# Optimization experiments

Hardware: AMD Instinct MI355X
Metric: run time of the kernel (lower is better)

The kernel has to match this reference:

```python
import jax, jax.numpy as jnp
import numpy as np

S, B, I, H, NQ = 256, 64, 512, 1024, 4


def setup_inputs() -> dict:
    key = jax.random.key(0)
    ks = jax.random.split(key, 12)
    w = lambda k, sh: jax.random.normal(k, sh, jnp.float32) * 0.05
    return {
        "inputs": jax.random.normal(ks[0], (S, B, I), jnp.float32),
        "Wf": w(ks[1], (I + H, H)), "bf": jnp.zeros((H,), jnp.float32),
        "Wi": w(ks[2], (I + H, H)), "bi": jnp.zeros((H,), jnp.float32),
        "Wu": w(ks[3], (I + H, H)), "bu": jnp.zeros((H,), jnp.float32),
        "Wo": w(ks[4], (I + H, H)), "bo": jnp.zeros((H,), jnp.float32),
        "pf": jax.random.normal(ks[5], (NQ,), jnp.float32),
        "pi_q": jax.random.normal(ks[6], (NQ,), jnp.float32),
        "pu": jax.random.normal(ks[7], (NQ,), jnp.float32),
        "po": jax.random.normal(ks[8], (NQ,), jnp.float32),
        "Wc": w(ks[9], (H + 1, H)), "bc": jnp.zeros((H,), jnp.float32),
    }


def reference(inputs, Wf, bf, Wi, bi, Wu, bu, Wo, bo, pf, pi_q, pu, po, Wc, bc):
    # inputs: (S, B, I); states initialized to zeros
    def qgate(pre, p):
        # pre: (B, H); use first NQ features -> simulated <Z> = cos(2*theta)
        theta = pre[:, :NQ] @ p  # (B,)
        return jnp.cos(2.0 * theta)[:, None]  # (B, 1)

    def comb(v):
        return v @ Wc + bc

    def step(carry, x):
        hx, cx = carry
        c = jnp.concatenate([x, hx], axis=1)  # (B, I+H)
        pre_f = c @ Wf + bf
        pre_i = c @ Wi + bi
        pre_u = c @ Wu + bu
        pre_o = c @ Wo + bo
        f = jax.nn.sigmoid(comb(jnp.concatenate(
            [jax.nn.sigmoid(pre_f), jax.nn.sigmoid(qgate(pre_f, pf))], axis=1)))
        i = jax.nn.sigmoid(comb(jnp.concatenate(
            [jax.nn.sigmoid(pre_i), jax.nn.sigmoid(qgate(pre_i, pi_q))], axis=1)))
        g = jnp.tanh(comb(jnp.concatenate(
            [jnp.tanh(pre_u), qgate(pre_u, pu)], axis=1)))  # update gate: no sigmoid on quantum part
        o = jax.nn.sigmoid(comb(jnp.concatenate(
            [jax.nn.sigmoid(pre_o), jax.nn.sigmoid(qgate(pre_o, po))], axis=1)))
        cx_new = f * cx + i * g
        hx_new = o * jnp.tanh(cx_new)
        return (hx_new, cx_new), hx_new

    init = (jnp.zeros((B, H), inputs.dtype), jnp.zeros((B, H), inputs.dtype))
    (hx, cx), outputs = jax.lax.scan(step, init, inputs)
    return outputs, (hx, cx)
```

## Files before the change

kernel.cpp:

```cpp
#include <hip/hip_runtime.h>

#define S_LEN 256
#define B_SZ 64
#define I_SZ 512
#define H_SZ 1024
#define NBLK 256

typedef __bf16 bf16x8 __attribute__((ext_vector_type(8)));
typedef float f32x4 __attribute__((ext_vector_type(4)));
typedef unsigned long long u64;

__device__ __forceinline__ float sigmoidf_(float x){ return 1.f/(1.f + expf(-x)); }

__device__ __forceinline__ u64 ld_cc64(const u64* p){
  return __hip_atomic_load(p, __ATOMIC_RELAXED, __HIP_MEMORY_SCOPE_AGENT);
}
__device__ __forceinline__ void st_cc16(__bf16* p, __bf16 v){
  unsigned short b = __builtin_bit_cast(unsigned short, v);
  __hip_atomic_store((unsigned short*)p, b, __ATOMIC_RELAXED, __HIP_MEMORY_SCOPE_AGENT);
}
__device__ __forceinline__ void st_cc32(float* p, float v){
  __hip_atomic_store(p, v, __ATOMIC_RELAXED, __HIP_MEMORY_SCOPE_AGENT);
}
__device__ __forceinline__ float ld_cc32f(const float* p){
  return __hip_atomic_load(p, __ATOMIC_RELAXED, __HIP_MEMORY_SCOPE_AGENT);
}


__global__ __launch_bounds__(64) void pack_w4_k(const float* __restrict__ Wf, const float* __restrict__ Wi,
                                                const float* __restrict__ Wu, const float* __restrict__ Wo,
                                                __bf16* __restrict__ W4p){
  int blk = blockIdx.x;
  int nt = blk / 48, kb = blk % 48;
  int l = threadIdx.x;
  int n = nt*16 + (l & 15);
  int g = n >> 10, h = n & 1023;
  const float* W = (g==0)?Wf:((g==1)?Wi:((g==2)?Wu:Wo));
  int k0 = kb*32 + ((l>>4)<<3);
  __bf16 tmp[8];
#pragma unroll
  for (int j=0;j<8;j++) tmp[j] = (__bf16)W[(size_t)(k0+j)*H_SZ + h];
  *reinterpret_cast<bf16x8*>(W4p + ((size_t)blk*64 + l)*8) = *reinterpret_cast<bf16x8*>(tmp);
}

__global__ __launch_bounds__(64) void pack_wc_k(const float* __restrict__ Wc, __bf16* __restrict__ Wcp){
  int blk = blockIdx.x;
  int nt = blk / 32, kb = blk % 32;
  int l = threadIdx.x;
  int n = nt*16 + (l & 15);
  int k0 = kb*32 + ((l>>4)<<3);
  __bf16 tmp[8];
#pragma unroll
  for (int j=0;j<8;j++) tmp[j] = (__bf16)Wc[(size_t)(k0+j)*H_SZ + n];
  *reinterpret_cast<bf16x8*>(Wcp + ((size_t)blk*64 + l)*8) = *reinterpret_cast<bf16x8*>(tmp);
}

__global__ __launch_bounds__(256) void pack_x_k(const float* __restrict__ x, __bf16* __restrict__ xF){
  int bid = blockIdx.x;
  int s = bid >> 2, mt = bid & 3;
#pragma unroll
  for (int j=0;j<4;j++){
    int G = j*256 + threadIdx.x;
    int kb = G >> 6, lane = G & 63;
    int b = mt*16 + (lane & 15);
    int k0 = kb*32 + ((lane>>4)<<3);
    const float* src = x + ((size_t)s*B_SZ + b)*I_SZ + k0;
    float4 v0 = *reinterpret_cast<const float4*>(src);
    float4 v1 = *reinterpret_cast<const float4*>(src+4);
    __bf16 t[8] = {(__bf16)v0.x,(__bf16)v0.y,(__bf16)v0.z,(__bf16)v0.w,
                   (__bf16)v1.x,(__bf16)v1.y,(__bf16)v1.z,(__bf16)v1.w};
    *reinterpret_cast<bf16x8*>(xF + ((size_t)bid*1024 + G)*8) = *reinterpret_cast<bf16x8*>(t);
  }
}

__global__ void init_h_k(__bf16* __restrict__ hxF){
  int i = blockIdx.x*blockDim.x + threadIdx.x;
  hxF[i] = (__bf16)0.f;
}

__device__ __forceinline__ void bar_arrive(unsigned* flags, unsigned target){
  asm volatile("" ::: "memory");
  __syncthreads();
  if (threadIdx.x == 0)
    __hip_atomic_store(&flags[blockIdx.x], target, __ATOMIC_RELAXED, __HIP_MEMORY_SCOPE_AGENT);
}
__device__ __forceinline__ void bar_wait(const unsigned* flags, unsigned target){
  if (threadIdx.x < 64){
    const u64* f = (const u64*)flags;
    int i0 = (int)threadIdx.x * 2;
    for(;;){
      u64 a = __hip_atomic_load(f+i0,   __ATOMIC_RELAXED, __HIP_MEMORY_SCOPE_AGENT);
      u64 b = __hip_atomic_load(f+i0+1, __ATOMIC_RELAXED, __HIP_MEMORY_SCOPE_AGENT);
      bool ok = ((unsigned)a >= target) && ((unsigned)(a>>32) >= target)
             && ((unsigned)b >= target) && ((unsigned)(b>>32) >= target);
      if (__all(ok)) break;
      __builtin_amdgcn_s_sleep(1);
    }
  }
  __syncthreads();
}


__global__ __launch_bounds__(256, 1) void qlstm_persist_k(
    const __bf16* __restrict__ xF,
    __bf16* hxF,
    const __bf16* __restrict__ W4p, const __bf16* __restrict__ Wcp,
    const float* __restrict__ bfv, const float* __restrict__ biv,
    const float* __restrict__ buv, const float* __restrict__ bov,
    const float* __restrict__ pf, const float* __restrict__ piq,
    const float* __restrict__ pu, const float* __restrict__ po,
    const float* __restrict__ WcLast, const float* __restrict__ bc,
    __bf16* actF, float* zact,
    float* __restrict__ out,
    unsigned* flags)
{
  __shared__ __align__(16) __bf16 ldsWc[2*32*64*8];
  __shared__ __align__(16) char ldsA[32768];
  __shared__ float gx[4][8][32];
  __shared__ float pre4[16][4];

  const int tid = threadIdx.x;
  const int bid = blockIdx.x;
  const int wave = tid >> 6;
  const int l = tid & 63;
  const int col = l & 15;
  const int kq = l >> 4;

  const int mt1 = bid >> 6;
  const int nt64 = bid & 63;
  const int nt16 = nt64*4 + wave;
  const int g1 = nt16 >> 6;
  const int h1 = (nt16*16 + col) & 1023;

  const int mt2 = bid >> 5;
  const int ht  = bid & 31;
  const int r2 = tid >> 5;
  const int c2 = tid & 31;
  const int b2 = mt2*8 + r2;
  const int h2 = ht*32 + c2;
  const int slot2 = kq*8 + (l & 7);

  bf16x8 wfrag[48];
  {
    const bf16x8* src = (const bf16x8*)(W4p + ((size_t)nt16*48*64 + (size_t)l)*8);
#pragma unroll
    for (int kb=0;kb<48;kb++) wfrag[kb] = src[(size_t)kb*64];
  }
  {
    const u64* src = (const u64*)(Wcp + (size_t)(ht*2)*32*64*8);
    u64* dst = (u64*)ldsWc;
    for (int i = tid; i < 8192; i += 256) dst[i] = src[i];
  }

  const float* bptr = (g1==0)?bfv:((g1==1)?biv:((g1==2)?buv:bov));
  const float bias1 = bptr[h1];
  const bool isU1 = (g1==2);
  const bool isQb = ((nt64 & 15) == 0);
  const int gq = nt64 >> 4;
  float pq0=0.f,pq1=0.f,pq2=0.f,pq3=0.f;
  if (isQb && wave==0){
    const float* pq = (gq==0)?pf:((gq==1)?piq:((gq==2)?pu:po));
    pq0=pq[0]; pq1=pq[1]; pq2=pq[2]; pq3=pq[3];
  }

  const float wl2 = WcLast[h2];
  const float bc2 = bc[h2];
  float creg = 0.f;

  const int laneh = (b2 & 15) + (((c2 >> 3) & 3) << 4);
  const size_t hei = ((size_t)((b2>>4)*32 + ht)*64 + laneh)*8 + (c2 & 7);

  __syncthreads();

  const size_t SBH = (size_t)S_LEN*B_SZ*H_SZ;

  for (int s = 0; s < S_LEN; ++s){
    {
      f32x4 acc[4] = {{0,0,0,0},{0,0,0,0},{0,0,0,0},{0,0,0,0}};
      const bf16x8* xp = (const bf16x8*)xF + (size_t)(s*4 + mt1)*1024 + l;
      {
        bf16x8 xf[8];
#pragma unroll
        for (int j=0;j<8;j++) xf[j] = xp[(size_t)j*64];
#pragma unroll
        for (int j=0;j<8;j++)
          acc[j&3] = __builtin_amdgcn_mfma_f32_16x16x32_bf16(xf[j], wfrag[j], acc[j&3], 0,0,0);
#pragma unroll
        for (int j=0;j<8;j++) xf[j] = xp[(size_t)(8+j)*64];
#pragma unroll
        for (int j=0;j<8;j++)
          acc[j&3] = __builtin_amdgcn_mfma_f32_16x16x32_bf16(xf[j], wfrag[8+j], acc[j&3], 0,0,0);
      }

      bar_wait(flags, (unsigned)(2*s));

      {
        const u64* hp = (const u64*)hxF + (size_t)mt1*4096;
        u64 slo[8], shi[8];
#pragma unroll
        for (int i=0;i<8;i++){
          int G = tid + 256*i;
          slo[i] = ld_cc64(hp + (size_t)G*2);
          shi[i] = ld_cc64(hp + (size_t)G*2 + 1);
        }
#pragma unroll
        for (int i=0;i<8;i++){
          int G = tid + 256*i;
          ulonglong2 v; v.x = slo[i]; v.y = shi[i];
          *reinterpret_cast<ulonglong2*>(ldsA + (size_t)G*16) = v;
        }
      }
      __syncthreads();

#pragma unroll
      for (int kb=0;kb<32;kb++){
        bf16x8 a = *reinterpret_cast<const bf16x8*>(ldsA + ((size_t)kb*64 + l)*16);
        acc[kb&3] = __builtin_amdgcn_mfma_f32_16x16x32_bf16(a, wfrag[16+kb], acc[kb&3], 0,0,0);
      }
      f32x4 r = (acc[0]+acc[1])+(acc[2]+acc[3]);
      float pr[4];
#pragma unroll
      for (int rr=0;rr<4;rr++){
        int brow = mt1*16 + (kq<<2) + rr;
        float p = r[rr] + bias1;
        pr[rr] = p;
        float a = isU1 ? tanhf(p) : sigmoidf_(p);
        size_t ei = (((size_t)(g1*8 + (brow>>3))*32 + (h1>>5))*32
                     + (size_t)((((h1>>3)&3)<<3) + (brow&7)))*8 + (h1&7);
        st_cc16(&actF[ei], (__bf16)a);
      }
      if (isQb && wave==0){
        if (col < 4){
#pragma unroll
          for (int rr=0;rr<4;rr++) pre4[(kq<<2)+rr][col] = pr[rr];
        }
        if (l < 16){
          float th = pre4[l][0]*pq0 + pre4[l][1]*pq1 + pre4[l][2]*pq2 + pre4[l][3]*pq3;
          float z = cosf(2.f*th);
          st_cc32(&zact[gq*B_SZ + mt1*16 + l], (gq==2) ? z : sigmoidf_(z));
        }
      }
    }

    bar_arrive(flags, (unsigned)(2*s+1));
    bar_wait(flags, (unsigned)(2*s+1));

    {
      float zf = ld_cc32f(&zact[      b2]);
      float zi = ld_cc32f(&zact[ 64 + b2]);
      float zu = ld_cc32f(&zact[128 + b2]);
      float zo = ld_cc32f(&zact[192 + b2]);

      const u64* ap = (const u64*)actF + (size_t)(wave*8 + mt2)*2048 + (size_t)slot2*2;
      const bf16x8* bf0 = (const bf16x8*)ldsWc + l;
      const bf16x8* bf1 = bf0 + 2048;
      f32x4 acc2[4] = {{0,0,0,0},{0,0,0,0},{0,0,0,0},{0,0,0,0}};
      u64 A0lo[8], A0hi[8], A1lo[8], A1hi[8];
#pragma unroll
      for (int i=0;i<8;i++){
        A0lo[i] = ld_cc64(ap + (size_t)i*64);
        A0hi[i] = ld_cc64(ap + (size_t)i*64 + 1);
      }
#pragma unroll
      for (int c=0;c<4;c++){
        u64* clo = (c&1) ? A1lo : A0lo;
        u64* chi = (c&1) ? A1hi : A0hi;
        u64* nlo = (c&1) ? A0lo : A1lo;
        u64* nhi = (c&1) ? A0hi : A1hi;
        if (c < 3){
#pragma unroll
          for (int i=0;i<8;i++){
            nlo[i] = ld_cc64(ap + (size_t)((c+1)*8 + i)*64);
            nhi[i] = ld_cc64(ap + (size_t)((c+1)*8 + i)*64 + 1);
          }
        }
#pragma unroll
        for (int i=0;i<8;i++){
          int kb = c*8 + i;
          union{u64 u[2]; bf16x8 v;} a; a.u[0]=clo[i]; a.u[1]=chi[i];
          acc2[kb&1]     = __builtin_amdgcn_mfma_f32_16x16x32_bf16(a.v, bf0[(size_t)kb*64], acc2[kb&1], 0,0,0);
          acc2[2+(kb&1)] = __builtin_amdgcn_mfma_f32_16x16x32_bf16(a.v, bf1[(size_t)kb*64], acc2[2+(kb&1)], 0,0,0);
        }
      }
      f32x4 rA = acc2[0]+acc2[1];
      f32x4 rB = acc2[2]+acc2[3];
#pragma unroll
      for (int rr=0;rr<4;rr++){
        int row = (kq<<2) + rr;
        if (row < 8){
          gx[wave][row][col]      = rA[rr];
          gx[wave][row][16 + col] = rB[rr];
        }
      }
      __syncthreads();

      float fg = sigmoidf_(gx[0][r2][c2] + bc2 + zf*wl2);
      float ig = sigmoidf_(gx[1][r2][c2] + bc2 + zi*wl2);
      float gg = tanhf(    gx[2][r2][c2] + bc2 + zu*wl2);
      float og = sigmoidf_(gx[3][r2][c2] + bc2 + zo*wl2);
      float cn = fg*creg + ig*gg;
      creg = cn;
      float hn = og*tanhf(cn);
      st_cc16(&hxF[hei], (__bf16)hn);
      size_t idx = (size_t)b2*H_SZ + h2;
      __builtin_nontemporal_store(hn, &out[(size_t)s*B_SZ*H_SZ + idx]);
      if (s == S_LEN-1){
        __builtin_nontemporal_store(hn, &out[SBH + idx]);
        __builtin_nontemporal_store(cn, &out[SBH + (size_t)B_SZ*H_SZ + idx]);
      }
    }

    bar_arrive(flags, (unsigned)(2*s+2));
  }
}


extern "C" void kernel_launch(void* const* d_in, const int* in_sizes, int n_in,
                              void* d_out, int out_size, void* d_ws, size_t ws_size,
                              hipStream_t stream){
  const float* inputs = (const float*)d_in[0];
  const float* Wf  = (const float*)d_in[1];
  const float* bf_ = (const float*)d_in[2];
  const float* Wi  = (const float*)d_in[3];
  const float* bi_ = (const float*)d_in[4];
  const float* Wu  = (const float*)d_in[5];
  const float* bu_ = (const float*)d_in[6];
  const float* Wo  = (const float*)d_in[7];
  const float* bo_ = (const float*)d_in[8];
  const float* pf  = (const float*)d_in[9];
  const float* piq = (const float*)d_in[10];
  const float* pu  = (const float*)d_in[11];
  const float* po  = (const float*)d_in[12];
  const float* Wc  = (const float*)d_in[13];
  const float* bc  = (const float*)d_in[14];
  float* out = (float*)d_out;

  __bf16* W4p = (__bf16*)d_ws;
  __bf16* Wcp = W4p + (size_t)256*48*64*8;
  __bf16* xF  = Wcp + (size_t)64*32*64*8;
  __bf16* actF = xF + (size_t)S_LEN*B_SZ*I_SZ;
  __bf16* hxF = actF + (size_t)4*B_SZ*H_SZ;
  float*  zact = (float*)(hxF + (size_t)B_SZ*H_SZ);
  unsigned* flags = (unsigned*)(zact + 256);

  pack_w4_k<<<256*48, 64, 0, stream>>>(Wf, Wi, Wu, Wo, W4p);
  pack_wc_k<<<64*32, 64, 0, stream>>>(Wc, Wcp);
  pack_x_k<<<S_LEN*4, 256, 0, stream>>>(inputs, xF);
  init_h_k<<<256, 256, 0, stream>>>(hxF);
  hipMemsetAsync(flags, 0, NBLK*sizeof(unsigned), stream);

  qlstm_persist_k<<<NBLK, 256, 0, stream>>>(
      xF, hxF, W4p, Wcp, bf_, bi_, bu_, bo_, pf, piq, pu, po,
      Wc + (size_t)H_SZ*H_SZ, bc, actF, zact, out, flags);
}
```

Baseline: 3.252 ms.

## Split grid barrier so phase-2 starts on first half of activations

Adds a three-phase per-step barrier. Blocks producing the second half of the gate activations signal early, once their hidden-state load is done. Phase-2 consumers begin the first half of their K-reduction after the intermediate barrier and wait for the full barrier only before reading the remaining activations. This is meant to overlap part of the combine GEMM with the tail of the gate GEMM and shorten the serial critical path per timestep. It also precomputes the activation store indices out of the loop. The change relies on an ordering assumption about which blocks write which activation halves, and it assumes that bar_wait/bar_arrive semantics (not shown) handle the new counter values correctly.

```diff
diff --git a/kernel.cpp b/kernel.cpp
--- a/kernel.cpp
+++ b/kernel.cpp
@@ -131,6 +131,7 @@
   const int nt16 = nt64*4 + wave;
   const int g1 = nt16 >> 6;
   const int h1 = (nt16*16 + col) & 1023;
+  const bool isHalfA = ((nt64 & 15) < 8);
 
   const int mt2 = bid >> 5;
   const int ht  = bid & 31;
@@ -167,6 +168,13 @@
   const float bc2 = bc[h2];
   float creg = 0.f;
 
+  size_t eis[4];
+#pragma unroll
+  for (int rr=0;rr<4;rr++){
+    int brow = mt1*16 + (kq<<2) + rr;
+    eis[rr] = (((size_t)(g1*8 + (brow>>3))*32 + (h1>>5))*32
+               + (size_t)((((h1>>3)&3)<<3) + (brow&7)))*8 + (h1&7);
+  }
   const int laneh = (b2 & 15) + (((c2 >> 3) & 3) << 4);
   const size_t hei = ((size_t)((b2>>4)*32 + ht)*64 + laneh)*8 + (c2 & 7);
 
@@ -175,6 +183,7 @@
   const size_t SBH = (size_t)S_LEN*B_SZ*H_SZ;
 
   for (int s = 0; s < S_LEN; ++s){
+    const unsigned T = 3u*(unsigned)s;
     {
       f32x4 acc[4] = {{0,0,0,0},{0,0,0,0},{0,0,0,0},{0,0,0,0}};
       const bf16x8* xp = (const bf16x8*)xF + (size_t)(s*4 + mt1)*1024 + l;
@@ -192,7 +201,7 @@
           acc[j&3] = __builtin_amdgcn_mfma_f32_16x16x32_bf16(xf[j], wfrag[8+j], acc[j&3], 0,0,0);
       }
 
-      bar_wait(flags, (unsigned)(2*s));
+      bar_wait(flags, T);
 
       {
         const u64* hp = (const u64*)hxF + (size_t)mt1*4096;
@@ -212,6 +221,9 @@
       }
       __syncthreads();
 
+      if (!isHalfA && tid == 0)
+        __hip_atomic_store(&flags[bid], T+1u, __ATOMIC_RELAXED, __HIP_MEMORY_SCOPE_AGENT);
+
 #pragma unroll
       for (int kb=0;kb<32;kb++){
         bf16x8 a = *reinterpret_cast<const bf16x8*>(ldsA + ((size_t)kb*64 + l)*16);
@@ -221,13 +233,10 @@
       float pr[4];
 #pragma unroll
       for (int rr=0;rr<4;rr++){
-        int brow = mt1*16 + (kq<<2) + rr;
         float p = r[rr] + bias1;
         pr[rr] = p;
         float a = isU1 ? tanhf(p) : sigmoidf_(p);
-        size_t ei = (((size_t)(g1*8 + (brow>>3))*32 + (h1>>5))*32
-                     + (size_t)((((h1>>3)&3)<<3) + (brow&7)))*8 + (h1&7);
-        st_cc16(&actF[ei], (__bf16)a);
+        st_cc16(&actF[eis[rr]], (__bf16)a);
       }
       if (isQb && wave==0){
         if (col < 4){
@@ -242,8 +251,8 @@
       }
     }
 
-    bar_arrive(flags, (unsigned)(2*s+1));
-    bar_wait(flags, (unsigned)(2*s+1));
+    bar_arrive(flags, T+2u);
+    bar_wait(flags, T+1u);
 
     {
       float zf = ld_cc32f(&zact[      b2]);
@@ -262,26 +271,51 @@
         A0hi[i] = ld_cc64(ap + (size_t)i*64 + 1);
       }
 #pragma unroll
-      for (int c=0;c<4;c++){
-        u64* clo = (c&1) ? A1lo : A0lo;
-        u64* chi = (c&1) ? A1hi : A0hi;
-        u64* nlo = (c&1) ? A0lo : A1lo;
-        u64* nhi = (c&1) ? A0hi : A1hi;
-        if (c < 3){
-#pragma unroll
-          for (int i=0;i<8;i++){
-            nlo[i] = ld_cc64(ap + (size_t)((c+1)*8 + i)*64);
-            nhi[i] = ld_cc64(ap + (size_t)((c+1)*8 + i)*64 + 1);
-          }
-        }
-#pragma unroll
-        for (int i=0;i<8;i++){
-          int kb = c*8 + i;
-          union{u64 u[2]; bf16x8 v;} a; a.u[0]=clo[i]; a.u[1]=chi[i];
-          acc2[kb&1]     = __builtin_amdgcn_mfma_f32_16x16x32_bf16(a.v, bf0[(size_t)kb*64], acc2[kb&1], 0,0,0);
-          acc2[2+(kb&1)] = __builtin_amdgcn_mfma_f32_16x16x32_bf16(a.v, bf1[(size_t)kb*64], acc2[2+(kb&1)], 0,0,0);
-        }
-      }
+      for (int i=0;i<8;i++){
+        A1lo[i] = ld_cc64(ap + (size_t)(8+i)*64);
+        A1hi[i] = ld_cc64(ap + (size_t)(8+i)*64 + 1);
+      }
+#pragma unroll
+      for (int i=0;i<8;i++){
+        union{u64 u[2]; bf16x8 v;} a; a.u[0]=A0lo[i]; a.u[1]=A0hi[i];
+        acc2[i&1]     = __builtin_amdgcn_mfma_f32_16x16x32_bf16(a.v, bf0[(size_t)i*64], acc2[i&1], 0,0,0);
+        acc2[2+(i&1)] = __builtin_amdgcn_mfma_f32_16x16x32_bf16(a.v, bf1[(size_t)i*64], acc2[2+(i&1)], 0,0,0);
+      }
+
+      bar_wait(flags, T+2u);
+
+#pragma unroll
+      for (int i=0;i<8;i++){
+        A0lo[i] = ld_cc64(ap + (size_t)(16+i)*64);
+        A0hi[i] = ld_cc64(ap + (size_t)(16+i)*64 + 1);
+      }
+#pragma unroll
+      for (int i=0;i<8;i++){
+        int kb = 8+i;
+        union{u64 u[2]; bf16x8 v;} a; a.u[0]=A1lo[i]; a.u[1]=A1hi[i];
+        acc2[kb&1]     = __builtin_amdgcn_mfma_f32_16x16x32_bf16(a.v, bf0[(size_t)kb*64], acc2[kb&1], 0,0,0);
+        acc2[2+(kb&1)] = __builtin_amdgcn_mfma_f32_16x16x32_bf16(a.v, bf1[(size_t)kb*64], acc2[2+(kb&1)], 0,0,0);
+      }
+#pragma unroll
+      for (int i=0;i<8;i++){
+        A1lo[i] = ld_cc64(ap + (size_t)(24+i)*64);
+        A1hi[i] = ld_cc64(ap + (size_t)(24+i)*64 + 1);
+      }
+#pragma unroll
+      for (int i=0;i<8;i++){
+        int kb = 16+i;
+        union{u64 u[2]; bf16x8 v;} a; a.u[0]=A0lo[i]; a.u[1]=A0hi[i];
+        acc2[kb&1]     = __builtin_amdgcn_mfma_f32_16x16x32_bf16(a.v, bf0[(size_t)kb*64], acc2[kb&1], 0,0,0);
+        acc2[2+(kb&1)] = __builtin_amdgcn_mfma_f32_16x16x32_bf16(a.v, bf1[(size_t)kb*64], acc2[2+(kb&1)], 0,0,0);
+      }
+#pragma unroll
+      for (int i=0;i<8;i++){
+        int kb = 24+i;
+        union{u64 u[2]; bf16x8 v;} a; a.u[0]=A1lo[i]; a.u[1]=A1hi[i];
+        acc2[kb&1]     = __builtin_amdgcn_mfma_f32_16x16x32_bf16(a.v, bf0[(size_t)kb*64], acc2[kb&1], 0,0,0);
+        acc2[2+(kb&1)] = __builtin_amdgcn_mfma_f32_16x16x32_bf16(a.v, bf1[(size_t)kb*64], acc2[2+(kb&1)], 0,0,0);
+      }
+
       f32x4 rA = acc2[0]+acc2[1];
       f32x4 rB = acc2[2]+acc2[3];
 #pragma unroll
@@ -310,7 +344,7 @@
       }
     }
 
-    bar_arrive(flags, (unsigned)(2*s+2));
+    bar_arrive(flags, T+3u);
   }
 }
 
```

After: 3.353 ms. +3.1%, slower.
